# Optimization experiments

Hardware: AMD Instinct MI355X
Metric: run time of the kernel (lower is better)

The kernel has to match this reference:

```python
import jax, jax.numpy as jnp
import numpy as np

EMBED_DIM = 1024
PROJ_DIM = 256


def setup_inputs() -> dict:
    key = jax.random.key(0)
    kx, kq, kk = jax.random.split(key, 3)
    x = jax.random.normal(kx, (8, 4096, EMBED_DIM), dtype=jnp.float32)
    scale = 1.0 / (PROJ_DIM ** 0.5)
    q_proj = jax.random.normal(kq, (EMBED_DIM, PROJ_DIM), dtype=jnp.float32) * scale
    k_proj = jax.random.normal(kk, (EMBED_DIM, PROJ_DIM), dtype=jnp.float32) * scale
    return {"x": x, "q_proj": q_proj, "k_proj": k_proj}


def reference(x, q_proj, k_proj):
    # exp feature maps (FAVOR-style)
    q_prime = jnp.exp(jnp.einsum('bld,de->ble', x, q_proj))  # [B, L, E]
    k_prime = jnp.exp(jnp.einsum('bld,de->ble', x, k_proj))  # [B, L, E]
    # associative KV summary: O(L*E*D)
    kv = jnp.einsum('ble,bld->bed', k_prime, x)               # [B, E, D]
    num = jnp.einsum('ble,bed->bld', q_prime, kv)             # [B, L, D]
    z = 1.0 / (jnp.sum(q_prime, axis=-1, keepdims=True) + 1e-8)
    return num * z
```

## Files before the change

kernel.cpp:

```cpp
#include <hip/hip_runtime.h>


#define EMBED 1024
#define PROJ  256
#define LSEQ  4096
#define BATCH 8

typedef short  bfrag __attribute__((ext_vector_type(8)));
typedef float  f4    __attribute__((ext_vector_type(4)));
typedef unsigned short u16x8 __attribute__((ext_vector_type(8)));
typedef unsigned short u16x4 __attribute__((ext_vector_type(4)));

static __device__ __forceinline__ unsigned short f2bf(float f) {
  unsigned int u = __builtin_bit_cast(unsigned int, f);
  u += 0x7fffu + ((u >> 16) & 1u);
  return (unsigned short)(u >> 16);
}
static __device__ __forceinline__ float bf2f(unsigned short h) {
  unsigned int u = ((unsigned int)h) << 16;
  return __builtin_bit_cast(float, u);
}

static __device__ __forceinline__ void gload_lds16(const void* g, void* l) {
  __builtin_amdgcn_global_load_lds(
      (__attribute__((address_space(1))) void*)(unsigned long long)(g),
      (__attribute__((address_space(3))) void*)(unsigned)(unsigned long long)(l),
      16, 0, 0);
}

static __device__ __forceinline__ void stage_tile(
    const unsigned short* __restrict__ src, int row0, int stride, int k0,
    unsigned short* lds, int wave, int lane) {
#pragma unroll
  for (int j = 0; j < 4; j++) {
    int slot = (wave * 4 + j) * 64 + lane;
    int r = slot >> 3, cp = slot & 7;
    int c = cp ^ (r & 7);
    gload_lds16(src + (size_t)(row0 + r) * stride + k0 + c * 8,
                lds + (wave * 4 + j) * 512);
  }
}

static __device__ __forceinline__ bfrag read_frag(const unsigned short* lds,
                                                  int row, int chunk) {
  return *(const bfrag*)(lds + ((row << 3) + (chunk ^ (row & 7))) * 8);
}

__global__ __launch_bounds__(256) void cvtx_kernel(
    const float* __restrict__ x, unsigned short* __restrict__ xb,
    unsigned short* __restrict__ xT) {
  __shared__ unsigned short T[64][72];
  const int tid = threadIdx.x;
  const int d0 = blockIdx.x * 64, l0 = blockIdx.y * 64, b = blockIdx.z;
#pragma unroll
  for (int it = 0; it < 4; it++) {
    int slot = it * 256 + tid;
    int r = slot >> 4, c4 = slot & 15;
    f4 v = *(const f4*)(x + ((size_t)(b * LSEQ + l0 + r)) * EMBED + d0 + c4 * 4);
    u16x4 h = (u16x4){f2bf(v[0]), f2bf(v[1]), f2bf(v[2]), f2bf(v[3])};
    *(u16x4*)(xb + ((size_t)(b * LSEQ + l0 + r)) * EMBED + d0 + c4 * 4) = h;
    T[c4 * 4 + 0][r] = h[0];
    T[c4 * 4 + 1][r] = h[1];
    T[c4 * 4 + 2][r] = h[2];
    T[c4 * 4 + 3][r] = h[3];
  }
  __syncthreads();
#pragma unroll
  for (int it = 0; it < 2; it++) {
    int slot = it * 256 + tid;
    int d = slot >> 3, ch = slot & 7;
    *(u16x8*)(xT + ((size_t)(b * EMBED + d0 + d)) * LSEQ + l0 + ch * 8) =
        *(const u16x8*)&T[d][ch * 8];
  }
}

__global__ __launch_bounds__(256) void cvtw_kernel(
    const float* __restrict__ qw, const float* __restrict__ kw,
    unsigned short* __restrict__ wt) {
  __shared__ unsigned short T[64][72];
  const int tid = threadIdx.x;
  const int n0 = blockIdx.x * 64, k0 = blockIdx.y * 64;
  const float* W = blockIdx.z ? kw : qw;
#pragma unroll
  for (int it = 0; it < 4; it++) {
    int slot = it * 256 + tid;
    int r = slot >> 4, c4 = slot & 15;
    f4 v = *(const f4*)(W + (size_t)(k0 + r) * PROJ + n0 + c4 * 4);
#pragma unroll
    for (int j = 0; j < 4; j++) T[c4 * 4 + j][r] = f2bf(v[j]);
  }
  __syncthreads();
#pragma unroll
  for (int it = 0; it < 2; it++) {
    int slot = it * 256 + tid;
    int n = slot >> 3, ch = slot & 7;
    *(u16x8*)(wt + ((size_t)(blockIdx.z * PROJ + n0 + n)) * EMBED + k0 + ch * 8) =
        *(const u16x8*)&T[n][ch * 8];
  }
}

__global__ __launch_bounds__(256) void proj_kernel(
    const unsigned short* __restrict__ xb, const unsigned short* __restrict__ wt,
    unsigned short* __restrict__ qp, unsigned short* __restrict__ kT) {
  __shared__ union {
    struct { unsigned short A[128 * 64]; unsigned short B[128 * 64]; } t;
    unsigned short T[128 * 136];
  } sm;
  const int tid = threadIdx.x, wave = tid >> 6, lane = tid & 63;
  const int quad = lane >> 4, l16 = lane & 15;
  const int wm = wave >> 1, wn = wave & 1;
  const int n0 = blockIdx.x * 128, m0 = blockIdx.y * 128;

  f4 acc[4][4];
#pragma unroll
  for (int i = 0; i < 4; i++)
#pragma unroll
    for (int j = 0; j < 4; j++) acc[i][j] = (f4){0.f, 0.f, 0.f, 0.f};

  for (int k0 = 0; k0 < EMBED; k0 += 64) {
    stage_tile(xb, m0, EMBED, k0, sm.t.A, wave, lane);
    stage_tile(wt, n0, EMBED, k0, sm.t.B, wave, lane);
    __syncthreads();
#pragma unroll
    for (int ks = 0; ks < 2; ks++) {
      bfrag a[4], bfr[4];
#pragma unroll
      for (int mt = 0; mt < 4; mt++)
        a[mt] = read_frag(sm.t.A, wm * 64 + mt * 16 + l16, ks * 4 + quad);
#pragma unroll
      for (int nt = 0; nt < 4; nt++)
        bfr[nt] = read_frag(sm.t.B, wn * 64 + nt * 16 + l16, ks * 4 + quad);
#pragma unroll
      for (int mt = 0; mt < 4; mt++)
#pragma unroll
        for (int nt = 0; nt < 4; nt++)
          acc[mt][nt] = __builtin_amdgcn_mfma_f32_16x16x32_bf16(
              a[mt], bfr[nt], acc[mt][nt], 0, 0, 0);
    }
    __syncthreads();
  }

  if (n0 < PROJ) {
#pragma unroll
    for (int mt = 0; mt < 4; mt++)
#pragma unroll
      for (int nt = 0; nt < 4; nt++)
#pragma unroll
        for (int r = 0; r < 4; r++)
          sm.T[(wm * 64 + mt * 16 + quad * 4 + r) * 136 + wn * 64 + nt * 16 + l16] =
              f2bf(__expf(acc[mt][nt][r]));
    __syncthreads();
#pragma unroll
    for (int it = 0; it < 8; it++) {
      int slot = it * 256 + tid;
      int row = slot >> 4, ch = slot & 15;
      *(u16x8*)(qp + (size_t)(m0 + row) * PROJ + n0 + ch * 8) =
          *(const u16x8*)&sm.T[row * 136 + ch * 8];
    }
  } else {
#pragma unroll
    for (int mt = 0; mt < 4; mt++)
#pragma unroll
      for (int nt = 0; nt < 4; nt++) {
        u16x4 h;
#pragma unroll
        for (int r = 0; r < 4; r++) h[r] = f2bf(__expf(acc[mt][nt][r]));
        *(u16x4*)&sm.T[(wn * 64 + nt * 16 + l16) * 136 + wm * 64 + mt * 16 + quad * 4] = h;
      }
    __syncthreads();
    const int bb = m0 >> 12, l0 = m0 & 4095, ebase = n0 - PROJ;
#pragma unroll
    for (int it = 0; it < 8; it++) {
      int slot = it * 256 + tid;
      int e = slot >> 4, ch = slot & 15;
      *(u16x8*)(kT + (size_t)(bb * PROJ + ebase + e) * LSEQ + l0 + ch * 8) =
          *(const u16x8*)&sm.T[e * 136 + ch * 8];
    }
  }
}

__global__ __launch_bounds__(256) void zinv_kernel(
    const unsigned short* __restrict__ qp, float* __restrict__ zinv) {
  int m = blockIdx.x * 4 + (threadIdx.x >> 6);
  int lane = threadIdx.x & 63;
  u16x4 h = *(const u16x4*)(qp + (size_t)m * PROJ + lane * 4);
  float s = bf2f(h[0]) + bf2f(h[1]) + bf2f(h[2]) + bf2f(h[3]);
#pragma unroll
  for (int off = 32; off; off >>= 1) s += __shfl_xor(s, off);
  if (lane == 0) zinv[m] = 1.0f / (s + 1e-8f);
}

__global__ __launch_bounds__(256) void kv_kernel(
    const unsigned short* __restrict__ kT, const unsigned short* __restrict__ xT,
    float* __restrict__ kvp) {
  __shared__ struct { unsigned short A[128 * 64]; unsigned short B[128 * 64]; } sm;
  const int tid = threadIdx.x, wave = tid >> 6, lane = tid & 63;
  const int quad = lane >> 4, l16 = lane & 15;
  const int wm = wave >> 1, wn = wave & 1;
  const int d0 = blockIdx.x * 128, e0 = blockIdx.y * 128;
  const int b = blockIdx.z & 7, split = blockIdx.z >> 3;
  const unsigned short* As = kT + (size_t)b * PROJ * LSEQ;
  const unsigned short* Bs = xT + (size_t)b * EMBED * LSEQ;

  f4 acc[4][4];
#pragma unroll
  for (int i = 0; i < 4; i++)
#pragma unroll
    for (int j = 0; j < 4; j++) acc[i][j] = (f4){0.f, 0.f, 0.f, 0.f};

  const int kbase = split * 512;
  for (int kk = 0; kk < 512; kk += 64) {
    stage_tile(As, e0, LSEQ, kbase + kk, sm.A, wave, lane);
    stage_tile(Bs, d0, LSEQ, kbase + kk, sm.B, wave, lane);
    __syncthreads();
#pragma unroll
    for (int ks = 0; ks < 2; ks++) {
      bfrag a[4], bfr[4];
#pragma unroll
      for (int mt = 0; mt < 4; mt++)
        a[mt] = read_frag(sm.A, wm * 64 + mt * 16 + l16, ks * 4 + quad);
#pragma unroll
      for (int nt = 0; nt < 4; nt++)
        bfr[nt] = read_frag(sm.B, wn * 64 + nt * 16 + l16, ks * 4 + quad);
#pragma unroll
      for (int mt = 0; mt < 4; mt++)
#pragma unroll
        for (int nt = 0; nt < 4; nt++)
          acc[mt][nt] = __builtin_amdgcn_mfma_f32_16x16x32_bf16(
              a[mt], bfr[nt], acc[mt][nt], 0, 0, 0);
    }
    __syncthreads();
  }

#pragma unroll
  for (int mt = 0; mt < 4; mt++)
#pragma unroll
    for (int nt = 0; nt < 4; nt++)
#pragma unroll
      for (int r = 0; r < 4; r++) {
        int e = e0 + wm * 64 + mt * 16 + quad * 4 + r;
        int d = d0 + wn * 64 + nt * 16 + l16;
        kvp[((size_t)(split * 8 + b) * PROJ + e) * EMBED + d] = acc[mt][nt][r];
      }
}

__global__ __launch_bounds__(256) void kvreduce_kernel(
    const float* __restrict__ kvp, unsigned short* __restrict__ kvT) {
  __shared__ float T[64][68];
  const int tid = threadIdx.x;
  const int d0 = blockIdx.x * 64, e0 = blockIdx.y * 64, b = blockIdx.z;
#pragma unroll
  for (int it = 0; it < 4; it++) {
    int slot = it * 256 + tid;
    int e = slot >> 4, c4 = slot & 15;
    f4 s = (f4){0.f, 0.f, 0.f, 0.f};
#pragma unroll
    for (int sp = 0; sp < 8; sp++)
      s += *(const f4*)(kvp + ((size_t)(sp * 8 + b) * PROJ + e0 + e) * EMBED + d0 + c4 * 4);
#pragma unroll
    for (int j = 0; j < 4; j++) T[c4 * 4 + j][e] = s[j];
  }
  __syncthreads();
#pragma unroll
  for (int it = 0; it < 2; it++) {
    int slot = it * 256 + tid;
    int d = slot >> 3, ch = slot & 7;
    u16x8 h;
#pragma unroll
    for (int j = 0; j < 8; j++) h[j] = f2bf(T[d][ch * 8 + j]);
    *(u16x8*)(kvT + ((size_t)(b * EMBED + d0 + d)) * PROJ + e0 + ch * 8) = h;
  }
}

__global__ __launch_bounds__(256) void out_kernel(
    const unsigned short* __restrict__ qp, const unsigned short* __restrict__ kvT,
    const float* __restrict__ zinv, float* __restrict__ out) {
  __shared__ struct { unsigned short A[128 * 64]; unsigned short B[128 * 64]; } sm;
  __shared__ float zv[128];
  const int tid = threadIdx.x, wave = tid >> 6, lane = tid & 63;
  const int quad = lane >> 4, l16 = lane & 15;
  const int wm = wave >> 1, wn = wave & 1;
  const int d0 = blockIdx.x * 128, l0 = blockIdx.y * 128, b = blockIdx.z;
  const unsigned short* As = qp + (size_t)b * LSEQ * PROJ;
  const unsigned short* Bs = kvT + (size_t)b * EMBED * PROJ;

  if (tid < 128) zv[tid] = zinv[b * LSEQ + l0 + tid];

  f4 acc[4][4];
#pragma unroll
  for (int i = 0; i < 4; i++)
#pragma unroll
    for (int j = 0; j < 4; j++) acc[i][j] = (f4){0.f, 0.f, 0.f, 0.f};

  for (int k0 = 0; k0 < PROJ; k0 += 64) {
    stage_tile(As, l0, PROJ, k0, sm.A, wave, lane);
    stage_tile(Bs, d0, PROJ, k0, sm.B, wave, lane);
    __syncthreads();
#pragma unroll
    for (int ks = 0; ks < 2; ks++) {
      bfrag a[4], bfr[4];
#pragma unroll
      for (int mt = 0; mt < 4; mt++)
        a[mt] = read_frag(sm.A, wm * 64 + mt * 16 + l16, ks * 4 + quad);
#pragma unroll
      for (int nt = 0; nt < 4; nt++)
        bfr[nt] = read_frag(sm.B, wn * 64 + nt * 16 + l16, ks * 4 + quad);
#pragma unroll
      for (int mt = 0; mt < 4; mt++)
#pragma unroll
        for (int nt = 0; nt < 4; nt++)
          acc[mt][nt] = __builtin_amdgcn_mfma_f32_16x16x32_bf16(
              a[mt], bfr[nt], acc[mt][nt], 0, 0, 0);
    }
    __syncthreads();
  }

#pragma unroll
  for (int mt = 0; mt < 4; mt++)
#pragma unroll
    for (int nt = 0; nt < 4; nt++)
#pragma unroll
      for (int r = 0; r < 4; r++) {
        int row = wm * 64 + mt * 16 + quad * 4 + r;
        int d = d0 + wn * 64 + nt * 16 + l16;
        out[((size_t)(b * LSEQ + l0 + row)) * EMBED + d] = acc[mt][nt][r] * zv[row];
      }
}

extern "C" void kernel_launch(void* const* d_in, const int* in_sizes, int n_in,
                              void* d_out, int out_size, void* d_ws, size_t ws_size,
                              hipStream_t stream) {
  const float* x  = (const float*)d_in[0];
  const float* qw = (const float*)d_in[1];
  const float* kw = (const float*)d_in[2];
  float* out = (float*)d_out;

  char* ws = (char*)d_ws;
  unsigned short* xb   = (unsigned short*)(ws);
  unsigned short* xT   = (unsigned short*)(ws + 67108864);
  unsigned short* wt   = (unsigned short*)(ws + 134217728);
  unsigned short* qp   = (unsigned short*)(ws + 135266304);
  unsigned short* kT   = (unsigned short*)(ws + 152043520);
  unsigned short* kvT  = (unsigned short*)(ws + 168820736);
  float*          zinv = (float*)(ws + 173015040);
  float*          kvp  = (float*)(ws);

  cvtx_kernel<<<dim3(16, 64, 8), 256, 0, stream>>>(x, xb, xT);
  cvtw_kernel<<<dim3(4, 16, 2), 256, 0, stream>>>(qw, kw, wt);
  proj_kernel<<<dim3(4, 256), 256, 0, stream>>>(xb, wt, qp, kT);
  zinv_kernel<<<dim3(8192), 256, 0, stream>>>(qp, zinv);
  kv_kernel<<<dim3(8, 2, 64), 256, 0, stream>>>(kT, xT, kvp);
  kvreduce_kernel<<<dim3(16, 4, 8), 256, 0, stream>>>(kvp, kvT);
  out_kernel<<<dim3(8, 32, 8), 256, 0, stream>>>(qp, kvT, zinv, out);
}
```

Before: 398.0 us.

## Swizzle cvtx transpose tile and halve kv split-K factor

The x conversion kernel now has each thread load four consecutive rows and write packed 4-element vectors into an XOR-swizzled LDS tile, in place of scalar stores into a padded array. This is meant to cut LDS bank conflicts and the number of shared-memory instructions in the transpose. Separately, the kv GEMM split-K drops from 8 to 4 splits with twice the K per block. That halves the partial-sum traffic written and then reduced, at the cost of fewer blocks (512) and so less parallelism.

```diff
diff --git a/kernel.cpp b/kernel.cpp
--- a/kernel.cpp
+++ b/kernel.cpp
@@ -49,28 +49,36 @@
 __global__ __launch_bounds__(256) void cvtx_kernel(
     const float* __restrict__ x, unsigned short* __restrict__ xb,
     unsigned short* __restrict__ xT) {
-  __shared__ unsigned short T[64][72];
+  __shared__ unsigned short T[64 * 64];
   const int tid = threadIdx.x;
   const int d0 = blockIdx.x * 64, l0 = blockIdx.y * 64, b = blockIdx.z;
-#pragma unroll
-  for (int it = 0; it < 4; it++) {
-    int slot = it * 256 + tid;
-    int r = slot >> 4, c4 = slot & 15;
-    f4 v = *(const f4*)(x + ((size_t)(b * LSEQ + l0 + r)) * EMBED + d0 + c4 * 4);
-    u16x4 h = (u16x4){f2bf(v[0]), f2bf(v[1]), f2bf(v[2]), f2bf(v[3])};
-    *(u16x4*)(xb + ((size_t)(b * LSEQ + l0 + r)) * EMBED + d0 + c4 * 4) = h;
-    T[c4 * 4 + 0][r] = h[0];
-    T[c4 * 4 + 1][r] = h[1];
-    T[c4 * 4 + 2][r] = h[2];
-    T[c4 * 4 + 3][r] = h[3];
+  const int br = tid & 15;
+  const int bcq = tid >> 4;
+
+  unsigned short h[4][4];
+#pragma unroll
+  for (int i = 0; i < 4; i++) {
+    const size_t row = (size_t)(b * LSEQ + l0 + br * 4 + i) * EMBED + d0 + bcq * 4;
+    f4 v = *(const f4*)(x + row);
+    u16x4 hv = (u16x4){f2bf(v[0]), f2bf(v[1]), f2bf(v[2]), f2bf(v[3])};
+    *(u16x4*)(xb + row) = hv;
+#pragma unroll
+    for (int k = 0; k < 4; k++) h[i][k] = hv[k];
+  }
+#pragma unroll
+  for (int k = 0; k < 4; k++) {
+    int dd = bcq * 4 + k;
+    int hp = br ^ ((dd & 7) << 1);
+    *(u16x4*)(T + dd * 64 + hp * 4) = (u16x4){h[0][k], h[1][k], h[2][k], h[3][k]};
   }
   __syncthreads();
 #pragma unroll
   for (int it = 0; it < 2; it++) {
     int slot = it * 256 + tid;
-    int d = slot >> 3, ch = slot & 7;
-    *(u16x8*)(xT + ((size_t)(b * EMBED + d0 + d)) * LSEQ + l0 + ch * 8) =
-        *(const u16x8*)&T[d][ch * 8];
+    int dd = slot >> 3, ch = slot & 7;
+    int cc = ch ^ (dd & 7);
+    *(u16x8*)(xT + ((size_t)(b * EMBED + d0 + dd)) * LSEQ + l0 + ch * 8) =
+        *(const u16x8*)(T + dd * 64 + cc * 8);
   }
 }
 
@@ -208,8 +216,8 @@
 #pragma unroll
     for (int j = 0; j < 4; j++) acc[i][j] = (f4){0.f, 0.f, 0.f, 0.f};
 
-  const int kbase = split * 512;
-  for (int kk = 0; kk < 512; kk += 64) {
+  const int kbase = split * 1024;
+  for (int kk = 0; kk < 1024; kk += 64) {
     stage_tile(As, e0, LSEQ, kbase + kk, sm.A, wave, lane);
     stage_tile(Bs, d0, LSEQ, kbase + kk, sm.B, wave, lane);
     __syncthreads();
@@ -255,7 +263,7 @@
     int e = slot >> 4, c4 = slot & 15;
     f4 s = (f4){0.f, 0.f, 0.f, 0.f};
 #pragma unroll
-    for (int sp = 0; sp < 8; sp++)
+    for (int sp = 0; sp < 4; sp++)
       s += *(const f4*)(kvp + ((size_t)(sp * 8 + b) * PROJ + e0 + e) * EMBED + d0 + c4 * 4);
 #pragma unroll
     for (int j = 0; j < 4; j++) T[c4 * 4 + j][e] = s[j];
@@ -349,7 +357,7 @@
   cvtw_kernel<<<dim3(4, 16, 2), 256, 0, stream>>>(qw, kw, wt);
   proj_kernel<<<dim3(4, 256), 256, 0, stream>>>(xb, wt, qp, kT);
   zinv_kernel<<<dim3(8192), 256, 0, stream>>>(qp, zinv);
-  kv_kernel<<<dim3(8, 2, 64), 256, 0, stream>>>(kT, xT, kvp);
+  kv_kernel<<<dim3(8, 2, 32), 256, 0, stream>>>(kT, xT, kvp);
   kvreduce_kernel<<<dim3(16, 4, 8), 256, 0, stream>>>(kvp, kvT);
   out_kernel<<<dim3(8, 32, 8), 256, 0, stream>>>(qp, kvT, zinv, out);
 }
```

Measured after the change: 390.6 us. No clear change (-1.9%).
